# Optimization experiments

Measured on AMD Instinct MI355X. Metric: run time of the kernel, lower is better.

Reference implementation:

```python
import jax, jax.numpy as jnp
import numpy as np


def gcn_layer(x, src, dst, W, b, n_dst):
    # DGL GraphConv, norm='both': D_src^{-1/2} pre-norm, sum aggregate, D_dst^{-1/2} post-norm, + bias
    n_src = x.shape[0]
    e_ones = jnp.ones(src.shape[0], dtype=x.dtype)
    deg_out = jnp.clip(jax.ops.segment_sum(e_ones, src, num_segments=n_src), 1.0)
    deg_in = jnp.clip(jax.ops.segment_sum(e_ones, dst, num_segments=n_dst), 1.0)
    h = (x * jax.lax.rsqrt(deg_out)[:, None]) @ W          # [n_src, out]
    agg = jax.ops.segment_sum(h[src], dst, num_segments=n_dst)  # [n_dst, out]
    return jax.nn.relu(agg * jax.lax.rsqrt(deg_in)[:, None] + b)


def setup_inputs() -> dict:
    key = jax.random.key(0)
    ks = jax.random.split(key, 8)
    N_SRC0, N_DST0, N_DST1 = 400000, 40000, 4000
    E0, E1 = 400000, 40000
    D_IN, D_HID, D_OUT = 256, 256, 256
    x = jax.random.normal(ks[0], (N_SRC0, D_IN), dtype=jnp.float32)
    src0 = jax.random.randint(ks[1], (E0,), 0, N_SRC0)
    dst0 = jax.random.randint(ks[2], (E0,), 0, N_DST0)
    src1 = jax.random.randint(ks[3], (E1,), 0, N_DST0)
    dst1 = jax.random.randint(ks[4], (E1,), 0, N_DST1)
    W0 = jax.random.normal(ks[5], (D_IN, D_HID), dtype=jnp.float32) * (1.0 / np.sqrt(D_IN))
    W1 = jax.random.normal(ks[6], (D_HID, D_OUT), dtype=jnp.float32) * (1.0 / np.sqrt(D_HID))
    b0 = jnp.zeros((D_HID,), dtype=jnp.float32)
    b1 = jnp.zeros((D_OUT,), dtype=jnp.float32)
    return {"x": x, "src0": src0, "dst0": dst0, "src1": src1, "dst1": dst1,
            "W0": W0, "b0": b0, "W1": W1, "b1": b1,
            "n_dst0": N_DST0, "n_dst1": N_DST1}


def reference(x, src0, dst0, src1, dst1, W0, b0, W1, b1, n_dst0, n_dst1):
    h = gcn_layer(x, src0, dst0, W0, b0, n_dst0)   # [n_dst0, hidden]
    out = gcn_layer(h, src1, dst1, W1, b1, n_dst1)  # [n_dst1, out]
    return out
```

## Files before the change

### kernel.cpp

```cpp
#include <hip/hip_runtime.h>
#include <hip/hip_bf16.h>
#include <cstddef>
#include <cstdint>


#define D 256
#define N_DST0_CONST 40000

typedef __attribute__((ext_vector_type(8))) short s16x8;
typedef __attribute__((ext_vector_type(4))) short s16x4;
typedef __attribute__((ext_vector_type(4))) float f32x4;

__device__ inline short f2bf(float f) {
    __hip_bfloat16 h = __float2bfloat16(f);
    return *reinterpret_cast<short*>(&h);
}

__global__ void zero_i(int* __restrict__ p, int n) {
    int i = blockIdx.x * blockDim.x + threadIdx.x;
    int stride = gridDim.x * blockDim.x;
    for (; i < n; i += stride) p[i] = 0;
}

__global__ __launch_bounds__(256) void count_deg_tr_both(
    const int* __restrict__ src0, const int* __restrict__ dst0, int E0,
    const int* __restrict__ src1, const int* __restrict__ dst1, int E1,
    int* __restrict__ cs0, int* __restrict__ cd0,
    int* __restrict__ cs1, int* __restrict__ cd1,
    int nEdgeBlocks,
    const float* __restrict__ Wa, short* __restrict__ BTa,
    const float* __restrict__ Wb, short* __restrict__ BTb) {
    int b = blockIdx.x;
    if (b < nEdgeBlocks) {
        int e = b * 256 + threadIdx.x;
        if (e < E0) {
            atomicAdd(&cs0[src0[e]], 1);
            atomicAdd(&cd0[dst0[e]], 1);
        } else if (e < E0 + E1) {
            int i = e - E0;
            atomicAdd(&cs1[src1[i]], 1);
            atomicAdd(&cd1[dst1[i]], 1);
        }
        return;
    }
    int t = b - nEdgeBlocks;
    const float* W = (t < 256) ? Wa : Wb;
    short* BT = (t < 256) ? BTa : BTb;
    t &= 255;
    int k0 = (t & 15) * 16;
    int n0 = (t >> 4) * 16;
    __shared__ float tile[16][17];
    int tx = threadIdx.x & 15, ty = threadIdx.x >> 4;
    tile[ty][tx] = W[(size_t)(k0 + ty) * D + n0 + tx];
    __syncthreads();
    BT[(size_t)(n0 + ty) * D + k0 + tx] = f2bf(tile[tx][ty]);
}

__global__ __launch_bounds__(1024) void ex_scan_both(
    const int* __restrict__ cnt0, int* __restrict__ ptr0, int n0,
    const int* __restrict__ cnt1, int* __restrict__ ptr1, int n1) {
    const int* cnt = (blockIdx.x == 0) ? cnt0 : cnt1;
    int* ptr = (blockIdx.x == 0) ? ptr0 : ptr1;
    int n = (blockIdx.x == 0) ? n0 : n1;

    __shared__ int wsum[16];
    const int tid = threadIdx.x;
    const int chunk = (n + 1023) / 1024;
    const int begin = min(tid * chunk, n);
    const int end = min(begin + chunk, n);
    int local = 0;
    for (int i = begin; i < end; ++i) local += cnt[i];
    const int lane = tid & 63;
    const int wid = tid >> 6;
    int v = local;
    for (int off = 1; off < 64; off <<= 1) {
        int u = __shfl_up(v, off, 64);
        if (lane >= off) v += u;
    }
    if (lane == 63) wsum[wid] = v;
    __syncthreads();
    if (wid == 0 && lane < 16) {
        int w = wsum[lane];
        for (int off = 1; off < 16; off <<= 1) {
            int u = __shfl_up(w, off, 16);
            if (lane >= off) w += u;
        }
        wsum[lane] = w;
    }
    __syncthreads();
    int base = (wid > 0 ? wsum[wid - 1] : 0) + (v - local);
    int run = base;
    for (int i = begin; i < end; ++i) { ptr[i] = run; run += cnt[i]; }
}

__global__ void fill_csr_both(const int* __restrict__ src0, const int* __restrict__ dst0, int E0,
                              const int* __restrict__ src1, const int* __restrict__ dst1, int E1,
                              int* __restrict__ ptr0, int* __restrict__ es0,
                              int* __restrict__ ptr1, int* __restrict__ es1) {
    int e = blockIdx.x * blockDim.x + threadIdx.x;
    if (e < E0) {
        int pos = atomicAdd(&ptr0[dst0[e]], 1);
        es0[pos] = src0[e];
    } else if (e < E0 + E1) {
        int i = e - E0;
        int pos = atomicAdd(&ptr1[dst1[i]], 1);
        es1[pos] = src1[i];
    }
}

__global__ __launch_bounds__(256) void gather_agg_bf16(
    const float* __restrict__ X, const int* __restrict__ edge_src,
    const int* __restrict__ ptr, const int* __restrict__ cnt_src,
    const int* __restrict__ needed,
    short* __restrict__ agg, int nrows) {
    int d = blockIdx.x * 4 + threadIdx.y;
    if (d >= nrows) return;
    if (needed && needed[d] == 0) return;
    int beg = (d == 0) ? 0 : ptr[d - 1];
    int end = ptr[d];
    int deg = end - beg;
    int lane = threadIdx.x;

    int s_l = 0;
    float rn_l = 0.f;
    if (lane < deg) {
        s_l = edge_src[beg + lane];
        rn_l = rsqrtf(fmaxf((float)cnt_src[s_l], 1.0f));
    }

    float4 acc = make_float4(0.f, 0.f, 0.f, 0.f);
    int nb = min(deg, 64);
    int j = 0;
    for (; j + 4 <= nb; j += 4) {
        int s0 = __shfl(s_l, j + 0), s1 = __shfl(s_l, j + 1);
        int s2 = __shfl(s_l, j + 2), s3 = __shfl(s_l, j + 3);
        float r0 = __shfl(rn_l, j + 0), r1 = __shfl(rn_l, j + 1);
        float r2 = __shfl(rn_l, j + 2), r3 = __shfl(rn_l, j + 3);
        float4 v0 = *(const float4*)(X + (size_t)s0 * D + lane * 4);
        float4 v1 = *(const float4*)(X + (size_t)s1 * D + lane * 4);
        float4 v2 = *(const float4*)(X + (size_t)s2 * D + lane * 4);
        float4 v3 = *(const float4*)(X + (size_t)s3 * D + lane * 4);
        acc.x += v0.x * r0 + v1.x * r1 + v2.x * r2 + v3.x * r3;
        acc.y += v0.y * r0 + v1.y * r1 + v2.y * r2 + v3.y * r3;
        acc.z += v0.z * r0 + v1.z * r1 + v2.z * r2 + v3.z * r3;
        acc.w += v0.w * r0 + v1.w * r1 + v2.w * r2 + v3.w * r3;
    }
    for (; j < nb; ++j) {
        int s = __shfl(s_l, j);
        float r = __shfl(rn_l, j);
        float4 v = *(const float4*)(X + (size_t)s * D + lane * 4);
        acc.x += v.x * r; acc.y += v.y * r; acc.z += v.z * r; acc.w += v.w * r;
    }
    for (int jj = beg + 64; jj < end; ++jj) {
        int s = edge_src[jj];
        float r = rsqrtf(fmaxf((float)cnt_src[s], 1.0f));
        float4 v = *(const float4*)(X + (size_t)s * D + lane * 4);
        acc.x += v.x * r; acc.y += v.y * r; acc.z += v.z * r; acc.w += v.w * r;
    }

    s16x4 o;
    o.x = f2bf(acc.x); o.y = f2bf(acc.y); o.z = f2bf(acc.z); o.w = f2bf(acc.w);
    *(s16x4*)(agg + (size_t)d * D + lane * 4) = o;
}

#define LDK 40

__global__ __launch_bounds__(256) void gemm_bf16_mfma(
    const short* __restrict__ A, const short* __restrict__ BT,
    const int* __restrict__ cnt_dst, const float* __restrict__ bias,
    float* __restrict__ out, int M) {
    __shared__ short As[128][LDK];
    __shared__ short Bs[128][LDK];

    const int tid = threadIdx.x;
    const int m0 = blockIdx.x * 128;
    const int n0 = blockIdx.y * 128;
    const int wave = tid >> 6;
    const int lane = tid & 63;
    const int l15 = lane & 15;
    const int quad = lane >> 4;
    const int mo = (wave & 1) * 64;
    const int no = (wave >> 1) * 64;

    f32x4 acc[4][4] = {};

    for (int k0 = 0; k0 < D; k0 += 32) {
#pragma unroll
        for (int i = 0; i < 2; ++i) {
            int idx = tid + i * 256;
            int row = idx >> 2;
            int kg = (idx & 3) * 8;
            int gm = m0 + row;
            s16x8 av = {};
            if (gm < M) av = *(const s16x8*)(A + (size_t)gm * D + k0 + kg);
            *(s16x8*)&As[row][kg] = av;
            s16x8 bv = *(const s16x8*)(BT + (size_t)(n0 + row) * D + k0 + kg);
            *(s16x8*)&Bs[row][kg] = bv;
        }
        __syncthreads();

        s16x8 af[4], bf[4];
#pragma unroll
        for (int mt = 0; mt < 4; ++mt)
            af[mt] = *(const s16x8*)&As[mo + mt * 16 + l15][quad * 8];
#pragma unroll
        for (int nt = 0; nt < 4; ++nt)
            bf[nt] = *(const s16x8*)&Bs[no + nt * 16 + l15][quad * 8];
#pragma unroll
        for (int mt = 0; mt < 4; ++mt)
#pragma unroll
            for (int nt = 0; nt < 4; ++nt)
                acc[mt][nt] = __builtin_amdgcn_mfma_f32_16x16x32_bf16(
                    af[mt], bf[nt], acc[mt][nt], 0, 0, 0);
        __syncthreads();
    }

#pragma unroll
    for (int mt = 0; mt < 4; ++mt) {
#pragma unroll
        for (int r = 0; r < 4; ++r) {
            int gm = m0 + mo + mt * 16 + quad * 4 + r;
            if (gm >= M) continue;
            float sc = rsqrtf(fmaxf((float)cnt_dst[gm], 1.0f));
#pragma unroll
            for (int nt = 0; nt < 4; ++nt) {
                int gn = n0 + no + nt * 16 + l15;
                float v = fmaxf(acc[mt][nt][r] * sc + bias[gn], 0.f);
                out[(size_t)gm * D + gn] = v;
            }
        }
    }
}


extern "C" void kernel_launch(void* const* d_in, const int* in_sizes, int n_in,
                              void* d_out, int out_size, void* d_ws, size_t ws_size,
                              hipStream_t stream) {
    const float* x    = (const float*)d_in[0];
    const int*   src0 = (const int*)d_in[1];
    const int*   dst0 = (const int*)d_in[2];
    const int*   src1 = (const int*)d_in[3];
    const int*   dst1 = (const int*)d_in[4];
    const float* W0   = (const float*)d_in[5];
    const float* b0   = (const float*)d_in[6];
    const float* W1   = (const float*)d_in[7];
    const float* b1   = (const float*)d_in[8];

    const int n_src0 = in_sizes[0] / D;
    const int E0     = in_sizes[1];
    const int E1     = in_sizes[3];
    const int n_dst0 = N_DST0_CONST;
    const int n_dst1 = out_size / D;

    char* base = (char*)d_ws;
    size_t off = 0;
    auto alloc = [&](size_t bytes) { void* p = base + off; off = (off + bytes + 63) & ~(size_t)63; return p; };

    int* icnt = (int*)alloc((size_t)(n_src0 + 2 * n_dst0 + n_dst1) * 4);
    int* icnt_src0 = icnt;
    int* icnt_dst0 = icnt + n_src0;
    int* icnt_src1 = icnt + n_src0 + n_dst0;
    int* icnt_dst1 = icnt + n_src0 + 2 * n_dst0;
    const int cnt_total = n_src0 + 2 * n_dst0 + n_dst1;

    int* ptr0      = (int*)alloc((size_t)n_dst0 * 4);
    int* ptr1      = (int*)alloc((size_t)n_dst1 * 4);
    int* edge_src0 = (int*)alloc((size_t)E0 * 4);
    int* edge_src1 = (int*)alloc((size_t)E1 * 4);

    float* h0    = (float*)alloc((size_t)n_dst0 * D * 4);
    short* aggb0 = (short*)alloc((size_t)n_dst0 * D * 2);
    short* aggb1 = (short*)alloc((size_t)n_dst1 * D * 2);
    short* BT0   = (short*)alloc((size_t)D * D * 2);
    short* BT1   = (short*)alloc((size_t)D * D * 2);

    float* out = (float*)d_out;

    zero_i<<<512, 256, 0, stream>>>(icnt, cnt_total);

    const int nEdgeBlocks = (E0 + E1 + 255) / 256;
    count_deg_tr_both<<<nEdgeBlocks + 512, 256, 0, stream>>>(
        src0, dst0, E0, src1, dst1, E1,
        icnt_src0, icnt_dst0, icnt_src1, icnt_dst1,
        nEdgeBlocks, W0, BT0, W1, BT1);

    ex_scan_both<<<2, 1024, 0, stream>>>(icnt_dst0, ptr0, n_dst0, icnt_dst1, ptr1, n_dst1);

    fill_csr_both<<<(E0 + E1 + 255) / 256, 256, 0, stream>>>(
        src0, dst0, E0, src1, dst1, E1, ptr0, edge_src0, ptr1, edge_src1);

    {
        dim3 blk(64, 4);
        gather_agg_bf16<<<(n_dst0 + 3) / 4, blk, 0, stream>>>(
            x, edge_src0, ptr0, icnt_src0, icnt_src1, aggb0, n_dst0);
        dim3 grid((n_dst0 + 127) / 128, D / 128);
        gemm_bf16_mfma<<<grid, 256, 0, stream>>>(aggb0, BT0, icnt_dst0, b0, h0, n_dst0);
    }

    {
        dim3 blk(64, 4);
        gather_agg_bf16<<<(n_dst1 + 3) / 4, blk, 0, stream>>>(
            h0, edge_src1, ptr1, icnt_src1, nullptr, aggb1, n_dst1);
        dim3 grid((n_dst1 + 127) / 128, D / 128);
        gemm_bf16_mfma<<<grid, 256, 0, stream>>>(aggb1, BT1, icnt_dst1, b1, out, n_dst1);
    }
}
```

Measured before the change: 672.6 us.

## Fuse gather-aggregate with MFMA GEMM per layer and store hidden layer in bf16

Merges the gather/aggregate kernel and the bf16 MFMA GEMM into one templated kernel. Each block aggregates a tile of destination rows into shared memory, then multiplies that tile by the transposed weights, which it reads straight from global memory. This removes the intermediate aggregate buffers and two launches. The hidden activation h0 is now stored as bf16, halving the layer-1 gather traffic at some precision cost. Rows outside the mask are also skipped in the layer-0 epilogue. Layer 1 uses small 16-row tiles to give more blocks.

```diff
diff --git a/kernel.cpp b/kernel.cpp
--- a/kernel.cpp
+++ b/kernel.cpp
@@ -6,6 +6,7 @@
 
 #define D 256
 #define N_DST0_CONST 40000
+#define LDSK 264
 
 typedef __attribute__((ext_vector_type(8))) short s16x8;
 typedef __attribute__((ext_vector_type(4))) short s16x4;
@@ -14,6 +15,10 @@
 __device__ inline short f2bf(float f) {
     __hip_bfloat16 h = __float2bfloat16(f);
     return *reinterpret_cast<short*>(&h);
+}
+__device__ inline float bf2f(short s) {
+    unsigned u = ((unsigned)(unsigned short)s) << 16;
+    return __uint_as_float(u);
 }
 
 __global__ void zero_i(int* __restrict__ p, int n) {
@@ -108,125 +113,135 @@
     }
 }
 
-__global__ __launch_bounds__(256) void gather_agg_bf16(
-    const float* __restrict__ X, const int* __restrict__ edge_src,
+template<bool XF32, bool OUTF32, int MT, bool USE_MASK>
+__global__ __launch_bounds__(256) void gcn_fused(
+    const void* __restrict__ Xv, const int* __restrict__ edge_src,
     const int* __restrict__ ptr, const int* __restrict__ cnt_src,
-    const int* __restrict__ needed,
-    short* __restrict__ agg, int nrows) {
-    int d = blockIdx.x * 4 + threadIdx.y;
-    if (d >= nrows) return;
-    if (needed && needed[d] == 0) return;
-    int beg = (d == 0) ? 0 : ptr[d - 1];
-    int end = ptr[d];
-    int deg = end - beg;
-    int lane = threadIdx.x;
-
-    int s_l = 0;
-    float rn_l = 0.f;
-    if (lane < deg) {
-        s_l = edge_src[beg + lane];
-        rn_l = rsqrtf(fmaxf((float)cnt_src[s_l], 1.0f));
-    }
-
-    float4 acc = make_float4(0.f, 0.f, 0.f, 0.f);
-    int nb = min(deg, 64);
-    int j = 0;
-    for (; j + 4 <= nb; j += 4) {
-        int s0 = __shfl(s_l, j + 0), s1 = __shfl(s_l, j + 1);
-        int s2 = __shfl(s_l, j + 2), s3 = __shfl(s_l, j + 3);
-        float r0 = __shfl(rn_l, j + 0), r1 = __shfl(rn_l, j + 1);
-        float r2 = __shfl(rn_l, j + 2), r3 = __shfl(rn_l, j + 3);
-        float4 v0 = *(const float4*)(X + (size_t)s0 * D + lane * 4);
-        float4 v1 = *(const float4*)(X + (size_t)s1 * D + lane * 4);
-        float4 v2 = *(const float4*)(X + (size_t)s2 * D + lane * 4);
-        float4 v3 = *(const float4*)(X + (size_t)s3 * D + lane * 4);
-        acc.x += v0.x * r0 + v1.x * r1 + v2.x * r2 + v3.x * r3;
-        acc.y += v0.y * r0 + v1.y * r1 + v2.y * r2 + v3.y * r3;
-        acc.z += v0.z * r0 + v1.z * r1 + v2.z * r2 + v3.z * r3;
-        acc.w += v0.w * r0 + v1.w * r1 + v2.w * r2 + v3.w * r3;
-    }
-    for (; j < nb; ++j) {
-        int s = __shfl(s_l, j);
-        float r = __shfl(rn_l, j);
-        float4 v = *(const float4*)(X + (size_t)s * D + lane * 4);
-        acc.x += v.x * r; acc.y += v.y * r; acc.z += v.z * r; acc.w += v.w * r;
-    }
-    for (int jj = beg + 64; jj < end; ++jj) {
-        int s = edge_src[jj];
-        float r = rsqrtf(fmaxf((float)cnt_src[s], 1.0f));
-        float4 v = *(const float4*)(X + (size_t)s * D + lane * 4);
-        acc.x += v.x * r; acc.y += v.y * r; acc.z += v.z * r; acc.w += v.w * r;
-    }
-
-    s16x4 o;
-    o.x = f2bf(acc.x); o.y = f2bf(acc.y); o.z = f2bf(acc.z); o.w = f2bf(acc.w);
-    *(s16x4*)(agg + (size_t)d * D + lane * 4) = o;
-}
-
-#define LDK 40
-
-__global__ __launch_bounds__(256) void gemm_bf16_mfma(
-    const short* __restrict__ A, const short* __restrict__ BT,
-    const int* __restrict__ cnt_dst, const float* __restrict__ bias,
-    float* __restrict__ out, int M) {
-    __shared__ short As[128][LDK];
-    __shared__ short Bs[128][LDK];
-
+    const int* __restrict__ needed, const int* __restrict__ cnt_dst,
+    const float* __restrict__ bias, const short* __restrict__ BT,
+    void* __restrict__ outv, int nrows) {
+    __shared__ short As[MT][LDSK];
     const int tid = threadIdx.x;
-    const int m0 = blockIdx.x * 128;
-    const int n0 = blockIdx.y * 128;
     const int wave = tid >> 6;
     const int lane = tid & 63;
+    const int m0 = blockIdx.x * MT;
+    constexpr int RPW = MT / 4;
+    constexpr int NMT = MT / 16;
+
+    const float* Xf = (const float*)Xv;
+    const short* Xh = (const short*)Xv;
+
+    for (int rr = 0; rr < RPW; ++rr) {
+        int row = wave * RPW + rr;
+        int d = m0 + row;
+        if (d >= nrows) break;
+        if (USE_MASK && needed[d] == 0) continue;
+        int beg = (d == 0) ? 0 : ptr[d - 1];
+        int end = ptr[d];
+        int deg = end - beg;
+
+        int s_l = 0;
+        float rn_l = 0.f;
+        if (lane < deg) {
+            s_l = edge_src[beg + lane];
+            rn_l = rsqrtf(fmaxf((float)cnt_src[s_l], 1.0f));
+        }
+
+        float4 acc = make_float4(0.f, 0.f, 0.f, 0.f);
+        int nb = min(deg, 64);
+        int j = 0;
+        for (; j + 4 <= nb; j += 4) {
+            int s0 = __shfl(s_l, j + 0), s1 = __shfl(s_l, j + 1);
+            int s2 = __shfl(s_l, j + 2), s3 = __shfl(s_l, j + 3);
+            float r0 = __shfl(rn_l, j + 0), r1 = __shfl(rn_l, j + 1);
+            float r2 = __shfl(rn_l, j + 2), r3 = __shfl(rn_l, j + 3);
+            float4 v0, v1, v2, v3;
+            if (XF32) {
+                v0 = *(const float4*)(Xf + (size_t)s0 * D + lane * 4);
+                v1 = *(const float4*)(Xf + (size_t)s1 * D + lane * 4);
+                v2 = *(const float4*)(Xf + (size_t)s2 * D + lane * 4);
+                v3 = *(const float4*)(Xf + (size_t)s3 * D + lane * 4);
+            } else {
+                s16x4 a = *(const s16x4*)(Xh + (size_t)s0 * D + lane * 4);
+                s16x4 b = *(const s16x4*)(Xh + (size_t)s1 * D + lane * 4);
+                s16x4 c = *(const s16x4*)(Xh + (size_t)s2 * D + lane * 4);
+                s16x4 e = *(const s16x4*)(Xh + (size_t)s3 * D + lane * 4);
+                v0 = make_float4(bf2f(a.x), bf2f(a.y), bf2f(a.z), bf2f(a.w));
+                v1 = make_float4(bf2f(b.x), bf2f(b.y), bf2f(b.z), bf2f(b.w));
+                v2 = make_float4(bf2f(c.x), bf2f(c.y), bf2f(c.z), bf2f(c.w));
+                v3 = make_float4(bf2f(e.x), bf2f(e.y), bf2f(e.z), bf2f(e.w));
+            }
+            acc.x += v0.x * r0 + v1.x * r1 + v2.x * r2 + v3.x * r3;
+            acc.y += v0.y * r0 + v1.y * r1 + v2.y * r2 + v3.y * r3;
+            acc.z += v0.z * r0 + v1.z * r1 + v2.z * r2 + v3.z * r3;
+            acc.w += v0.w * r0 + v1.w * r1 + v2.w * r2 + v3.w * r3;
+        }
+        for (; j < nb; ++j) {
+            int s = __shfl(s_l, j);
+            float r = __shfl(rn_l, j);
+            float4 v;
+            if (XF32) {
+                v = *(const float4*)(Xf + (size_t)s * D + lane * 4);
+            } else {
+                s16x4 a = *(const s16x4*)(Xh + (size_t)s * D + lane * 4);
+                v = make_float4(bf2f(a.x), bf2f(a.y), bf2f(a.z), bf2f(a.w));
+            }
+            acc.x += v.x * r; acc.y += v.y * r; acc.z += v.z * r; acc.w += v.w * r;
+        }
+        for (int jj = beg + 64; jj < end; ++jj) {
+            int s = edge_src[jj];
+            float r = rsqrtf(fmaxf((float)cnt_src[s], 1.0f));
+            float4 v;
+            if (XF32) {
+                v = *(const float4*)(Xf + (size_t)s * D + lane * 4);
+            } else {
+                s16x4 a = *(const s16x4*)(Xh + (size_t)s * D + lane * 4);
+                v = make_float4(bf2f(a.x), bf2f(a.y), bf2f(a.z), bf2f(a.w));
+            }
+            acc.x += v.x * r; acc.y += v.y * r; acc.z += v.z * r; acc.w += v.w * r;
+        }
+
+        s16x4 o;
+        o.x = f2bf(acc.x); o.y = f2bf(acc.y); o.z = f2bf(acc.z); o.w = f2bf(acc.w);
+        *(s16x4*)&As[row][lane * 4] = o;
+    }
+    __syncthreads();
+
     const int l15 = lane & 15;
     const int quad = lane >> 4;
-    const int mo = (wave & 1) * 64;
-    const int no = (wave >> 1) * 64;
-
-    f32x4 acc[4][4] = {};
-
+    const int n0w = wave * 64;
+
+    f32x4 acc[NMT][4] = {};
     for (int k0 = 0; k0 < D; k0 += 32) {
-#pragma unroll
-        for (int i = 0; i < 2; ++i) {
-            int idx = tid + i * 256;
-            int row = idx >> 2;
-            int kg = (idx & 3) * 8;
-            int gm = m0 + row;
-            s16x8 av = {};
-            if (gm < M) av = *(const s16x8*)(A + (size_t)gm * D + k0 + kg);
-            *(s16x8*)&As[row][kg] = av;
-            s16x8 bv = *(const s16x8*)(BT + (size_t)(n0 + row) * D + k0 + kg);
-            *(s16x8*)&Bs[row][kg] = bv;
-        }
-        __syncthreads();
-
-        s16x8 af[4], bf[4];
-#pragma unroll
-        for (int mt = 0; mt < 4; ++mt)
-            af[mt] = *(const s16x8*)&As[mo + mt * 16 + l15][quad * 8];
+        s16x8 af[NMT], bfr[4];
 #pragma unroll
         for (int nt = 0; nt < 4; ++nt)
-            bf[nt] = *(const s16x8*)&Bs[no + nt * 16 + l15][quad * 8];
-#pragma unroll
-        for (int mt = 0; mt < 4; ++mt)
+            bfr[nt] = *(const s16x8*)(BT + (size_t)(n0w + nt * 16 + l15) * D + k0 + quad * 8);
+#pragma unroll
+        for (int mt = 0; mt < NMT; ++mt)
+            af[mt] = *(const s16x8*)&As[mt * 16 + l15][k0 + quad * 8];
+#pragma unroll
+        for (int mt = 0; mt < NMT; ++mt)
 #pragma unroll
             for (int nt = 0; nt < 4; ++nt)
                 acc[mt][nt] = __builtin_amdgcn_mfma_f32_16x16x32_bf16(
-                    af[mt], bf[nt], acc[mt][nt], 0, 0, 0);
-        __syncthreads();
-    }
-
-#pragma unroll
-    for (int mt = 0; mt < 4; ++mt) {
+                    af[mt], bfr[nt], acc[mt][nt], 0, 0, 0);
+    }
+
+#pragma unroll
+    for (int mt = 0; mt < NMT; ++mt) {
 #pragma unroll
         for (int r = 0; r < 4; ++r) {
-            int gm = m0 + mo + mt * 16 + quad * 4 + r;
-            if (gm >= M) continue;
+            int gm = m0 + mt * 16 + quad * 4 + r;
+            if (gm >= nrows) continue;
+            if (USE_MASK && needed[gm] == 0) continue;
             float sc = rsqrtf(fmaxf((float)cnt_dst[gm], 1.0f));
 #pragma unroll
             for (int nt = 0; nt < 4; ++nt) {
-                int gn = n0 + no + nt * 16 + l15;
+                int gn = n0w + nt * 16 + l15;
                 float v = fmaxf(acc[mt][nt][r] * sc + bias[gn], 0.f);
-                out[(size_t)gm * D + gn] = v;
+                if (OUTF32) ((float*)outv)[(size_t)gm * D + gn] = v;
+                else        ((short*)outv)[(size_t)gm * D + gn] = f2bf(v);
             }
         }
     }
@@ -268,11 +283,9 @@
     int* edge_src0 = (int*)alloc((size_t)E0 * 4);
     int* edge_src1 = (int*)alloc((size_t)E1 * 4);
 
-    float* h0    = (float*)alloc((size_t)n_dst0 * D * 4);
-    short* aggb0 = (short*)alloc((size_t)n_dst0 * D * 2);
-    short* aggb1 = (short*)alloc((size_t)n_dst1 * D * 2);
-    short* BT0   = (short*)alloc((size_t)D * D * 2);
-    short* BT1   = (short*)alloc((size_t)D * D * 2);
+    short* h0b = (short*)alloc((size_t)n_dst0 * D * 2);
+    short* BT0 = (short*)alloc((size_t)D * D * 2);
+    short* BT1 = (short*)alloc((size_t)D * D * 2);
 
     float* out = (float*)d_out;
 
@@ -289,19 +302,9 @@
     fill_csr_both<<<(E0 + E1 + 255) / 256, 256, 0, stream>>>(
         src0, dst0, E0, src1, dst1, E1, ptr0, edge_src0, ptr1, edge_src1);
 
-    {
-        dim3 blk(64, 4);
-        gather_agg_bf16<<<(n_dst0 + 3) / 4, blk, 0, stream>>>(
-            x, edge_src0, ptr0, icnt_src0, icnt_src1, aggb0, n_dst0);
-        dim3 grid((n_dst0 + 127) / 128, D / 128);
-        gemm_bf16_mfma<<<grid, 256, 0, stream>>>(aggb0, BT0, icnt_dst0, b0, h0, n_dst0);
-    }
-
-    {
-        dim3 blk(64, 4);
-        gather_agg_bf16<<<(n_dst1 + 3) / 4, blk, 0, stream>>>(
-            h0, edge_src1, ptr1, icnt_src1, nullptr, aggb1, n_dst1);
-        dim3 grid((n_dst1 + 127) / 128, D / 128);
-        gemm_bf16_mfma<<<grid, 256, 0, stream>>>(aggb1, BT1, icnt_dst1, b1, out, n_dst1);
-    }
-}
+    gcn_fused<true, false, 64, true><<<(n_dst0 + 63) / 64, 256, 0, stream>>>(
+        x, edge_src0, ptr0, icnt_src0, icnt_src1, icnt_dst0, b0, BT0, h0b, n_dst0);
+
+    gcn_fused<false, true, 16, false><<<(n_dst1 + 15) / 16, 256, 0, stream>>>(
+        h0b, edge_src1, ptr1, icnt_src1, nullptr, icnt_dst1, b1, BT1, out, n_dst1);
+}
```

After: 674.3 us. Within noise of the previous version (+0.3%).
